# Kernel tuning notes

Measured on AMD Instinct MI355X. Metric: run time of the kernel, lower is better.

The kernel has to match this reference:

```python
import jax, jax.numpy as jnp
import numpy as np

D = 64       # CNF state dimension
H = 512      # MLP hidden width
B = 8192     # batch


def setup_inputs() -> dict:
    key = jax.random.key(0)
    ks = jax.random.split(key, 8)
    s1 = 1.0 / np.sqrt(D + 1)
    s2 = 1.0 / np.sqrt(H)
    return {
        "t": jax.random.uniform(ks[0], (1,), dtype=jnp.float32),
        "x": jax.random.normal(ks[1], (B, D + 1), dtype=jnp.float32),
        "W1": jax.random.normal(ks[2], (D + 1, H), dtype=jnp.float32) * s1,
        "b1": jnp.zeros((H,), dtype=jnp.float32),
        "W2": jax.random.normal(ks[3], (H, H), dtype=jnp.float32) * s2,
        "b2": jnp.zeros((H,), dtype=jnp.float32),
        "W3": jax.random.normal(ks[4], (H, D), dtype=jnp.float32) * s2,
        "b3": jnp.zeros((D,), dtype=jnp.float32),
    }


def reference(t, x, W1, b1, W2, b2, W3, b3):
    # CNF.forward: strip log-density channel, evaluate vf and its exact divergence.
    xs = x[..., :-1]                      # [B, D]
    tt = t[0]

    def vf_single(xi):                    # xi: [D] -> [D]
        inp = jnp.concatenate([tt[None], xi])          # vf(t*ones, x) with t prepended
        h = jnp.tanh(inp @ W1 + b1)
        h = jnp.tanh(h @ W2 + b2)
        return h @ W3 + b3

    dx = jax.vmap(vf_single)(xs)                        # [B, D]
    # exact divergence: trace of per-sample Jacobian via reverse-mode (matches torch jacrev)
    J = jax.vmap(jax.jacrev(vf_single))(xs)             # [B, D, D]
    div = jnp.trace(J, axis1=-2, axis2=-1)              # [B]
    return jnp.concatenate([dx, div[:, None]], axis=-1) # [B, D+1]
```

## Files before the change

kernel.cpp:

```cpp
#include <hip/hip_runtime.h>

#define HH 512
#define DD 64
#define MROWS 32
#define TPB 512
#define LP 520

typedef unsigned short u16;
typedef short s16x8 __attribute__((ext_vector_type(8)));
typedef float f32x4 __attribute__((ext_vector_type(4)));

#define MFMA16(A,B,C) __builtin_amdgcn_mfma_f32_16x16x32_bf16((A),(B),(C),0,0,0)

#define OFF_W2K  0
#define OFF_EFK  262144
#define OFF_W1F  524288
#define OFF_W3F  557056
#define OFF_Z0B  (589824 * 2)

__device__ __forceinline__ u16 f2bf(float f) {
    unsigned u = __builtin_bit_cast(unsigned, f);
    u += 0x7fffu + ((u >> 16) & 1u);
    return (u16)(u >> 16);
}
__device__ __forceinline__ float bf2f(u16 h) {
    return __builtin_bit_cast(float, (unsigned)h << 16);
}
__device__ __forceinline__ float fast_tanh(float x) {
    float e = __expf(2.0f * x);
    return 1.0f - 2.0f * __builtin_amdgcn_rcpf(e + 1.0f);
}
__device__ __forceinline__ void gll(const u16* g, u16* l) {
    __builtin_amdgcn_global_load_lds(
        (const __attribute__((address_space(1))) unsigned int*)g,
        (__attribute__((address_space(3))) unsigned int*)l, 16, 0, 0);
}
__device__ __forceinline__ void wait_vm4() {
    asm volatile("s_waitcnt vmcnt(4)" ::: "memory");
}
__device__ __forceinline__ void wait_vm0() {
    asm volatile("s_waitcnt vmcnt(0)" ::: "memory");
}
__device__ __forceinline__ void fence_lds_reads() {
    asm volatile("s_waitcnt lgkmcnt(0)" ::: "memory");
}

__global__ __launch_bounds__(256) void precompute(
    const float* __restrict__ t,  const float* __restrict__ W1,
    const float* __restrict__ b1, const float* __restrict__ W2,
    const float* __restrict__ W3, u16* __restrict__ ws16, float* __restrict__ z0)
{
    __shared__ float T[16 * 264 > 256 * 20 ? 16 * 264 : 256 * 20];
    u16* W2K = ws16 + OFF_W2K;
    u16* EFK = ws16 + OFF_EFK;
    u16* W1F = ws16 + OFF_W1F;
    u16* W3F = ws16 + OFF_W3F;

    const int bid = blockIdx.x, tid = threadIdx.x;
    const int lane = tid & 63, wv = tid >> 6;
    const int m16 = lane & 15, q = lane >> 4;

    if (bid < 64) {
        const int nt = bid >> 1, bh = bid & 1;
        const int a0 = nt * 16, b0 = bh * 256;
        s16x8 afh[2], afl[2];
#pragma unroll
        for (int h = 0; h < 2; ++h)
#pragma unroll
            for (int j = 0; j < 8; ++j) {
                int i = h * 32 + q * 8 + j;
                float v = W1[(1 + i) * HH + a0 + m16];
                u16 hi = f2bf(v);
                afh[h][j] = (short)hi;
                afl[h][j] = (short)f2bf(v - bf2f(hi));
            }
#pragma unroll
        for (int bt = 0; bt < 4; ++bt) {
            int bl = wv * 64 + bt * 16;
            s16x8 bfh[2], bfl[2];
#pragma unroll
            for (int h = 0; h < 2; ++h) {
                const float* src = W3 + (b0 + bl + m16) * DD + h * 32 + q * 8;
                float4 p0 = *(const float4*)(src);
                float4 p1 = *(const float4*)(src + 4);
                float vv[8] = {p0.x,p0.y,p0.z,p0.w,p1.x,p1.y,p1.z,p1.w};
#pragma unroll
                for (int j = 0; j < 8; ++j) {
                    u16 hi = f2bf(vv[j]);
                    bfh[h][j] = (short)hi;
                    bfl[h][j] = (short)f2bf(vv[j] - bf2f(hi));
                }
            }
            f32x4 c = {0.f, 0.f, 0.f, 0.f};
#pragma unroll
            for (int h = 0; h < 2; ++h) {
                c = MFMA16(afh[h], bfh[h], c);
                c = MFMA16(afh[h], bfl[h], c);
                c = MFMA16(afl[h], bfh[h], c);
            }
#pragma unroll
            for (int r = 0; r < 4; ++r)
                T[(4 * q + r) * 264 + bl + m16] = c[r];
        }
        __syncthreads();
#pragma unroll
        for (int p = 0; p < 2; ++p) {
            int ksl = p * 4 + wv;
            int al  = m16;
            int blc = ksl * 32 + q * 8;
            const float* w2p = W2 + (a0 + al) * HH + b0 + blc;
            float4 wa = *(const float4*)(w2p), wb = *(const float4*)(w2p + 4);
            const float* glp = T + al * 264 + blc;
            s16x8 o;
            o[0]=(short)f2bf(wa.x*glp[0]); o[1]=(short)f2bf(wa.y*glp[1]);
            o[2]=(short)f2bf(wa.z*glp[2]); o[3]=(short)f2bf(wa.w*glp[3]);
            o[4]=(short)f2bf(wb.x*glp[4]); o[5]=(short)f2bf(wb.y*glp[5]);
            o[6]=(short)f2bf(wb.z*glp[6]); o[7]=(short)f2bf(wb.w*glp[7]);
            *(s16x8*)(EFK + (b0 / 32 + ksl) * 16384 + nt * 512 + lane * 8) = o;
        }
        if (bh == 0 && tid < 128) {
            int ks = tid >> 6, ln = tid & 63;
            int n  = nt * 16 + (ln & 15);
            int k0 = ks * 32 + (ln >> 4) * 8;
            s16x8 o;
#pragma unroll
            for (int j = 0; j < 8; ++j) o[j] = (short)f2bf(W1[(1 + k0 + j) * HH + n]);
            *(s16x8*)(W1F + nt * 1024 + ks * 512 + ln * 8) = o;
        }
    } else if (bid < 128) {
        const int nt = (bid - 64) >> 1, kh = (bid - 64) & 1;
        const int n0 = nt * 16, k0 = kh * 256;
#pragma unroll
        for (int it = 0; it < 4; ++it) {
            int r = (tid >> 2) + it * 64;
            int c = (tid & 3) * 4;
            float4 v = *(const float4*)(W2 + (k0 + r) * HH + n0 + c);
            *(float4*)(T + r * 20 + c) = v;
        }
        __syncthreads();
#pragma unroll
        for (int p = 0; p < 2; ++p) {
            int ksl = p * 4 + wv;
            int kqx = ksl * 32 + q * 8;
            s16x8 o;
#pragma unroll
            for (int j = 0; j < 8; ++j) o[j] = (short)f2bf(T[(kqx + j) * 20 + m16]);
            *(s16x8*)(W2K + (k0 / 32 + ksl) * 16384 + nt * 512 + lane * 8) = o;
        }
    } else if (bid < 136) {
        const int ot = (bid - 128) >> 1, kh = (bid - 128) & 1;
        const int o0 = ot * 16, k0 = kh * 256;
#pragma unroll
        for (int it = 0; it < 4; ++it) {
            int r = (tid >> 2) + it * 64;
            int c = (tid & 3) * 4;
            float4 v = *(const float4*)(W3 + (k0 + r) * DD + o0 + c);
            *(float4*)(T + r * 20 + c) = v;
        }
        __syncthreads();
#pragma unroll
        for (int p = 0; p < 2; ++p) {
            int ksl = p * 4 + wv;
            int kqx = ksl * 32 + q * 8;
            s16x8 o;
#pragma unroll
            for (int j = 0; j < 8; ++j) o[j] = (short)f2bf(T[(kqx + j) * 20 + m16]);
            *(s16x8*)(W3F + ot * 8192 + (k0 / 32 + ksl) * 512 + lane * 8) = o;
        }
    } else {
        for (int n = tid; n < HH; n += 256)
            z0[n] = b1[n] + t[0] * W1[n];
    }
}

__global__ __launch_bounds__(TPB) void cnf_main(
    const float* __restrict__ x,  const u16* __restrict__ ws16,
    const float* __restrict__ z0, const float* __restrict__ b2,
    const float* __restrict__ b3, float* __restrict__ out)
{
    __shared__ u16 h1s[MROWS * LP];
    __shared__ u16 h2s[MROWS * LP];
    __shared__ u16 stg[2][16384];
    __shared__ float z0s[HH];
    __shared__ float b2s[HH];
    __shared__ float b3s[DD];
    __shared__ float divacc[8][MROWS];

    const u16* W2K = ws16 + OFF_W2K;
    const u16* EFK = ws16 + OFF_EFK;
    const u16* W1F = ws16 + OFF_W1F;
    const u16* W3F = ws16 + OFF_W3F;

    const int tid  = threadIdx.x;
    const int lane = tid & 63;
    const int w    = tid >> 6;
    const int m16  = lane & 15;
    const int q    = lane >> 4;
    const int kq   = q * 8;
    const int r0   = blockIdx.x * MROWS;

    u16* xs = h2s;

#pragma unroll
    for (int j = 0; j < 4; ++j)
        gll(W2K + (4 * w + j) * 512 + lane * 8,         stg[0] + w * 2048 + j * 512);
#pragma unroll
    for (int j = 0; j < 4; ++j)
        gll(W2K + 16384 + (4 * w + j) * 512 + lane * 8, stg[1] + w * 2048 + j * 512);

    for (int idx = tid; idx < MROWS * DD; idx += TPB) {
        int r = idx >> 6, c = idx & 63;
        xs[r * 72 + c] = f2bf(x[(r0 + r) * (DD + 1) + c]);
    }
    z0s[tid] = z0[tid];
    b2s[tid] = b2[tid];
    if (tid < DD) b3s[tid] = b3[tid];

    s16x8 b1f[4][2];
#pragma unroll
    for (int j = 0; j < 4; ++j) {
        const u16* bb = W1F + (4 * w + j) * 1024 + lane * 8;
        b1f[j][0] = *(const s16x8*)(bb);
        b1f[j][1] = *(const s16x8*)(bb + 512);
    }
    __syncthreads();

    float d1reg[2][4][4];

    {
        s16x8 xa[2][2];
#pragma unroll
        for (int rt = 0; rt < 2; ++rt) {
            xa[rt][0] = *(const s16x8*)(xs + (rt * 16 + m16) * 72 + kq);
            xa[rt][1] = *(const s16x8*)(xs + (rt * 16 + m16) * 72 + 32 + kq);
        }
#pragma unroll
        for (int j = 0; j < 4; ++j) {
            int col = (4 * w + j) * 16 + m16;
#pragma unroll
            for (int rt = 0; rt < 2; ++rt) {
                f32x4 c = {0.f, 0.f, 0.f, 0.f};
                c = MFMA16(xa[rt][0], b1f[j][0], c);
                c = MFMA16(xa[rt][1], b1f[j][1], c);
#pragma unroll
                for (int i = 0; i < 4; ++i) {
                    float hv = fast_tanh(c[i] + z0s[col]);
                    h1s[(rt * 16 + 4 * q + i) * LP + col] = f2bf(hv);
                    d1reg[rt][j][i] = 1.0f - hv * hv;
                }
            }
        }
    }
    __syncthreads();

    f32x4 acc[2][4];
#pragma unroll
    for (int rt = 0; rt < 2; ++rt)
#pragma unroll
        for (int j = 0; j < 4; ++j) acc[rt][j] = f32x4{0.f,0.f,0.f,0.f};
    {
        const u16* ap0 = h1s + m16 * LP + kq;
        const u16* ap1 = h1s + (16 + m16) * LP + kq;
#pragma unroll 4
        for (int c = 0; c < 16; ++c) {
            if (c < 15) wait_vm4(); else wait_vm0();
            u16* sb = stg[c & 1] + w * 2048;
            s16x8 bf0 = *(const s16x8*)(sb +        lane * 8);
            s16x8 bf1 = *(const s16x8*)(sb +  512 + lane * 8);
            s16x8 bf2 = *(const s16x8*)(sb + 1024 + lane * 8);
            s16x8 bf3 = *(const s16x8*)(sb + 1536 + lane * 8);
            s16x8 f0  = *(const s16x8*)(ap0 + c * 32);
            s16x8 f1  = *(const s16x8*)(ap1 + c * 32);
            acc[0][0] = MFMA16(f0, bf0, acc[0][0]);
            acc[1][0] = MFMA16(f1, bf0, acc[1][0]);
            acc[0][1] = MFMA16(f0, bf1, acc[0][1]);
            acc[1][1] = MFMA16(f1, bf1, acc[1][1]);
            acc[0][2] = MFMA16(f0, bf2, acc[0][2]);
            acc[1][2] = MFMA16(f1, bf2, acc[1][2]);
            acc[0][3] = MFMA16(f0, bf3, acc[0][3]);
            acc[1][3] = MFMA16(f1, bf3, acc[1][3]);
            if (c < 14) {
                fence_lds_reads();
                const u16* src = W2K + (c + 2) * 16384 + 4 * w * 512 + lane * 8;
#pragma unroll
                for (int j = 0; j < 4; ++j) gll(src + j * 512, sb + j * 512);
            }
        }
    }

    fence_lds_reads();
#pragma unroll
    for (int j = 0; j < 4; ++j)
        gll(EFK + (4 * w + j) * 512 + lane * 8,         stg[0] + w * 2048 + j * 512);
#pragma unroll
    for (int j = 0; j < 4; ++j)
        gll(EFK + 16384 + (4 * w + j) * 512 + lane * 8, stg[1] + w * 2048 + j * 512);

#pragma unroll
    for (int j = 0; j < 4; ++j) {
        int col = (4 * w + j) * 16 + m16;
#pragma unroll
        for (int rt = 0; rt < 2; ++rt)
#pragma unroll
            for (int i = 0; i < 4; ++i)
                h2s[(rt * 16 + 4 * q + i) * LP + col] =
                    f2bf(fast_tanh(acc[rt][j][i] + b2s[col]));
    }
    __syncthreads();

    {
        const int rowt = w >> 2, ot = w & 3;
        const u16* ap = h2s + (rowt * 16 + m16) * LP + kq;
        const u16* bp = W3F + ot * 8192 + lane * 8;
        s16x8 W3r[4];
#pragma unroll
        for (int k = 0; k < 4; ++k) W3r[k] = *(const s16x8*)(bp + k * 512);
        f32x4 cA = {0.f,0.f,0.f,0.f}, cB = {0.f,0.f,0.f,0.f};
#pragma unroll
        for (int c = 0; c < 16; ++c) {
            s16x8 f = *(const s16x8*)(ap + c * 32);
            const int sl = c & 3;
            if (c & 1) cB = MFMA16(f, W3r[sl], cB);
            else       cA = MFMA16(f, W3r[sl], cA);
            if (c < 12) W3r[sl] = *(const s16x8*)(bp + (c + 4) * 512);
        }
        f32x4 c3 = cA + cB;
        int o = ot * 16 + m16;
#pragma unroll
        for (int i = 0; i < 4; ++i)
            out[(r0 + rowt * 16 + 4 * q + i) * (DD + 1) + o] = c3[i] + b3s[o];
    }

    {
        f32x4 g[2][4];
#pragma unroll
        for (int rt = 0; rt < 2; ++rt)
#pragma unroll
            for (int j = 0; j < 4; ++j) g[rt][j] = f32x4{0.f,0.f,0.f,0.f};
        const u16* ap0 = h2s + m16 * LP + kq;
        const u16* ap1 = h2s + (16 + m16) * LP + kq;
#pragma unroll 4
        for (int c = 0; c < 16; ++c) {
            if (c < 15) wait_vm4(); else wait_vm0();
            u16* sb = stg[c & 1] + w * 2048;
            s16x8 ef0 = *(const s16x8*)(sb +        lane * 8);
            s16x8 ef1 = *(const s16x8*)(sb +  512 + lane * 8);
            s16x8 ef2 = *(const s16x8*)(sb + 1024 + lane * 8);
            s16x8 ef3 = *(const s16x8*)(sb + 1536 + lane * 8);
            s16x8 hf0 = *(const s16x8*)(ap0 + c * 32);
            s16x8 hf1 = *(const s16x8*)(ap1 + c * 32);
            s16x8 af0, af1;
#pragma unroll
            for (int jj = 0; jj < 8; ++jj) {
                float v0 = bf2f((u16)hf0[jj]);
                float v1 = bf2f((u16)hf1[jj]);
                af0[jj] = (short)f2bf(1.0f - v0 * v0);
                af1[jj] = (short)f2bf(1.0f - v1 * v1);
            }
            g[0][0] = MFMA16(af0, ef0, g[0][0]);
            g[1][0] = MFMA16(af1, ef0, g[1][0]);
            g[0][1] = MFMA16(af0, ef1, g[0][1]);
            g[1][1] = MFMA16(af1, ef1, g[1][1]);
            g[0][2] = MFMA16(af0, ef2, g[0][2]);
            g[1][2] = MFMA16(af1, ef2, g[1][2]);
            g[0][3] = MFMA16(af0, ef3, g[0][3]);
            g[1][3] = MFMA16(af1, ef3, g[1][3]);
            if (c < 14) {
                fence_lds_reads();
                const u16* src = EFK + (c + 2) * 16384 + 4 * w * 512 + lane * 8;
#pragma unroll
                for (int j = 0; j < 4; ++j) gll(src + j * 512, sb + j * 512);
            }
        }
#pragma unroll
        for (int rt = 0; rt < 2; ++rt)
#pragma unroll
            for (int i = 0; i < 4; ++i) {
                float v = d1reg[rt][0][i] * g[rt][0][i]
                        + d1reg[rt][1][i] * g[rt][1][i]
                        + d1reg[rt][2][i] * g[rt][2][i]
                        + d1reg[rt][3][i] * g[rt][3][i];
                v += __shfl_xor(v, 1, 64);
                v += __shfl_xor(v, 2, 64);
                v += __shfl_xor(v, 4, 64);
                v += __shfl_xor(v, 8, 64);
                if (m16 == 0) divacc[w][rt * 16 + 4 * q + i] = v;
            }
    }
    __syncthreads();

    if (tid < MROWS) {
        float s = 0.0f;
#pragma unroll
        for (int ww = 0; ww < 8; ++ww) s += divacc[ww][tid];
        out[(r0 + tid) * (DD + 1) + DD] = s;
    }
}

extern "C" void kernel_launch(void* const* d_in, const int* in_sizes, int n_in,
                              void* d_out, int out_size, void* d_ws, size_t ws_size,
                              hipStream_t stream) {
    const float* t  = (const float*)d_in[0];
    const float* x  = (const float*)d_in[1];
    const float* W1 = (const float*)d_in[2];
    const float* b1 = (const float*)d_in[3];
    const float* W2 = (const float*)d_in[4];
    const float* b2 = (const float*)d_in[5];
    const float* W3 = (const float*)d_in[6];
    const float* b3 = (const float*)d_in[7];
    float* out = (float*)d_out;

    u16*   ws16 = (u16*)d_ws;
    float* z0   = (float*)((char*)d_ws + OFF_Z0B);

    precompute<<<137, 256, 0, stream>>>(t, W1, b1, W2, W3, ws16, z0);
    cnf_main<<<8192 / MROWS, TPB, 0, stream>>>(x, ws16, z0, b2, b3, out);
}
```

Before: 96.82 us.

## Split fused CNF kernel into four staged kernels with larger GEMM tiles

The single fused kernel is replaced by four kernels: layer-1 (writing h1 and d1 to workspace in MFMA-fragment layout), a 128x128-tiled W2 GEMM producing h2 and its tanh derivative, a 128x128-tiled divergence GEMM against EFK, and an output kernel for W3 that also sums the partial divergences. Larger tiles are meant to raise weight reuse, since each 32-row block previously streamed all of W2 and EFK. The cost is extra launches and global round-trips of intermediates (h1, h2, d2, d1), roughly tens of MB of traffic, plus less per-block parallelism with only 256 blocks of 256 threads.

```diff
diff --git a/kernel.cpp b/kernel.cpp
--- a/kernel.cpp
+++ b/kernel.cpp
@@ -2,9 +2,6 @@
 
 #define HH 512
 #define DD 64
-#define MROWS 32
-#define TPB 512
-#define LP 520
 
 typedef unsigned short u16;
 typedef short s16x8 __attribute__((ext_vector_type(8)));
@@ -17,6 +14,11 @@
 #define OFF_W1F  524288
 #define OFF_W3F  557056
 #define OFF_Z0B  (589824 * 2)
+#define OFF_H1T_B (2u*1024*1024)
+#define OFF_H2T_B (12u*1024*1024)
+#define OFF_D2T_B (22u*1024*1024)
+#define OFF_D1_B  (32u*1024*1024)
+#define OFF_PD_B  (42u*1024*1024)
 
 __device__ __forceinline__ u16 f2bf(float f) {
     unsigned u = __builtin_bit_cast(unsigned, f);
@@ -34,15 +36,6 @@
     __builtin_amdgcn_global_load_lds(
         (const __attribute__((address_space(1))) unsigned int*)g,
         (__attribute__((address_space(3))) unsigned int*)l, 16, 0, 0);
-}
-__device__ __forceinline__ void wait_vm4() {
-    asm volatile("s_waitcnt vmcnt(4)" ::: "memory");
-}
-__device__ __forceinline__ void wait_vm0() {
-    asm volatile("s_waitcnt vmcnt(0)" ::: "memory");
-}
-__device__ __forceinline__ void fence_lds_reads() {
-    asm volatile("s_waitcnt lgkmcnt(0)" ::: "memory");
 }
 
 __global__ __launch_bounds__(256) void precompute(
@@ -173,49 +166,24 @@
     }
 }
 
-__global__ __launch_bounds__(TPB) void cnf_main(
-    const float* __restrict__ x,  const u16* __restrict__ ws16,
-    const float* __restrict__ z0, const float* __restrict__ b2,
-    const float* __restrict__ b3, float* __restrict__ out)
+__global__ __launch_bounds__(512) void k1_h1(
+    const float* __restrict__ x, const u16* __restrict__ ws16,
+    const float* __restrict__ z0, u16* __restrict__ h1t, u16* __restrict__ d1)
 {
-    __shared__ u16 h1s[MROWS * LP];
-    __shared__ u16 h2s[MROWS * LP];
-    __shared__ u16 stg[2][16384];
+    __shared__ u16 h1s[32 * 520];
+    __shared__ u16 xs[32 * 72];
     __shared__ float z0s[HH];
-    __shared__ float b2s[HH];
-    __shared__ float b3s[DD];
-    __shared__ float divacc[8][MROWS];
-
-    const u16* W2K = ws16 + OFF_W2K;
-    const u16* EFK = ws16 + OFF_EFK;
+
     const u16* W1F = ws16 + OFF_W1F;
-    const u16* W3F = ws16 + OFF_W3F;
-
-    const int tid  = threadIdx.x;
-    const int lane = tid & 63;
-    const int w    = tid >> 6;
-    const int m16  = lane & 15;
-    const int q    = lane >> 4;
-    const int kq   = q * 8;
-    const int r0   = blockIdx.x * MROWS;
-
-    u16* xs = h2s;
-
-#pragma unroll
-    for (int j = 0; j < 4; ++j)
-        gll(W2K + (4 * w + j) * 512 + lane * 8,         stg[0] + w * 2048 + j * 512);
-#pragma unroll
-    for (int j = 0; j < 4; ++j)
-        gll(W2K + 16384 + (4 * w + j) * 512 + lane * 8, stg[1] + w * 2048 + j * 512);
-
-    for (int idx = tid; idx < MROWS * DD; idx += TPB) {
+    const int tid = threadIdx.x, lane = tid & 63, w = tid >> 6;
+    const int m16 = lane & 15, q = lane >> 4, kq = q * 8;
+    const int r0 = blockIdx.x * 32;
+
+    for (int idx = tid; idx < 32 * DD; idx += 512) {
         int r = idx >> 6, c = idx & 63;
         xs[r * 72 + c] = f2bf(x[(r0 + r) * (DD + 1) + c]);
     }
     z0s[tid] = z0[tid];
-    b2s[tid] = b2[tid];
-    if (tid < DD) b3s[tid] = b3[tid];
-
     s16x8 b1f[4][2];
 #pragma unroll
     for (int j = 0; j < 4; ++j) {
@@ -225,8 +193,6 @@
     }
     __syncthreads();
 
-    float d1reg[2][4][4];
-
     {
         s16x8 xa[2][2];
 #pragma unroll
@@ -245,155 +211,225 @@
 #pragma unroll
                 for (int i = 0; i < 4; ++i) {
                     float hv = fast_tanh(c[i] + z0s[col]);
-                    h1s[(rt * 16 + 4 * q + i) * LP + col] = f2bf(hv);
-                    d1reg[rt][j][i] = 1.0f - hv * hv;
+                    h1s[(rt * 16 + 4 * q + i) * 520 + col] = f2bf(hv);
+                    d1[(r0 + rt * 16 + 4 * q + i) * HH + col] = f2bf(1.0f - hv * hv);
                 }
             }
         }
     }
     __syncthreads();
 
-    f32x4 acc[2][4];
-#pragma unroll
-    for (int rt = 0; rt < 2; ++rt)
-#pragma unroll
-        for (int j = 0; j < 4; ++j) acc[rt][j] = f32x4{0.f,0.f,0.f,0.f};
-    {
-        const u16* ap0 = h1s + m16 * LP + kq;
-        const u16* ap1 = h1s + (16 + m16) * LP + kq;
-#pragma unroll 4
-        for (int c = 0; c < 16; ++c) {
-            if (c < 15) wait_vm4(); else wait_vm0();
-            u16* sb = stg[c & 1] + w * 2048;
-            s16x8 bf0 = *(const s16x8*)(sb +        lane * 8);
-            s16x8 bf1 = *(const s16x8*)(sb +  512 + lane * 8);
-            s16x8 bf2 = *(const s16x8*)(sb + 1024 + lane * 8);
-            s16x8 bf3 = *(const s16x8*)(sb + 1536 + lane * 8);
-            s16x8 f0  = *(const s16x8*)(ap0 + c * 32);
-            s16x8 f1  = *(const s16x8*)(ap1 + c * 32);
-            acc[0][0] = MFMA16(f0, bf0, acc[0][0]);
-            acc[1][0] = MFMA16(f1, bf0, acc[1][0]);
-            acc[0][1] = MFMA16(f0, bf1, acc[0][1]);
-            acc[1][1] = MFMA16(f1, bf1, acc[1][1]);
-            acc[0][2] = MFMA16(f0, bf2, acc[0][2]);
-            acc[1][2] = MFMA16(f1, bf2, acc[1][2]);
-            acc[0][3] = MFMA16(f0, bf3, acc[0][3]);
-            acc[1][3] = MFMA16(f1, bf3, acc[1][3]);
-            if (c < 14) {
-                fence_lds_reads();
-                const u16* src = W2K + (c + 2) * 16384 + 4 * w * 512 + lane * 8;
-#pragma unroll
-                for (int j = 0; j < 4; ++j) gll(src + j * 512, sb + j * 512);
-            }
-        }
-    }
-
-    fence_lds_reads();
-#pragma unroll
-    for (int j = 0; j < 4; ++j)
-        gll(EFK + (4 * w + j) * 512 + lane * 8,         stg[0] + w * 2048 + j * 512);
-#pragma unroll
-    for (int j = 0; j < 4; ++j)
-        gll(EFK + 16384 + (4 * w + j) * 512 + lane * 8, stg[1] + w * 2048 + j * 512);
-
-#pragma unroll
-    for (int j = 0; j < 4; ++j) {
-        int col = (4 * w + j) * 16 + m16;
-#pragma unroll
-        for (int rt = 0; rt < 2; ++rt)
-#pragma unroll
-            for (int i = 0; i < 4; ++i)
-                h2s[(rt * 16 + 4 * q + i) * LP + col] =
-                    f2bf(fast_tanh(acc[rt][j][i] + b2s[col]));
+    const int rowblk = blockIdx.x >> 2;
+#pragma unroll
+    for (int p = 0; p < 2; ++p) {
+        int ch = 2 * w + p;
+#pragma unroll
+        for (int rt = 0; rt < 2; ++rt) {
+            int rtg = (blockIdx.x & 3) * 2 + rt;
+            s16x8 f = *(const s16x8*)(h1s + (rt * 16 + m16) * 520 + ch * 32 + kq);
+            *(s16x8*)(h1t + (rowblk * 16 + ch) * 4096 + rtg * 512 + lane * 8) = f;
+        }
+    }
+}
+
+__global__ __launch_bounds__(256) void k2_h2(
+    const u16* __restrict__ ws16, const u16* __restrict__ h1t,
+    const float* __restrict__ b2, u16* __restrict__ h2t, u16* __restrict__ d2t)
+{
+    __shared__ u16 smem[16384];
+
+    const u16* W2K = ws16 + OFF_W2K;
+    const int tid = threadIdx.x, lane = tid & 63, w = tid >> 6;
+    const int m16 = lane & 15, q = lane >> 4, kq = q * 8;
+    const int rowblk = blockIdx.x >> 2, ng = blockIdx.x & 3;
+    const int rh = w >> 1, nh = w & 1;
+
+    const u16* habase = h1t + rowblk * 16 * 4096;
+
+#pragma unroll
+    for (int s = 0; s < 2; ++s) {
+        gll(habase + (w + 4 * s) * 512 + lane * 8, smem + (w + 4 * s) * 512);
+        gll(W2K + (ng * 8 + w + 4 * s) * 512 + lane * 8, smem + 4096 + (w + 4 * s) * 512);
     }
     __syncthreads();
 
-    {
-        const int rowt = w >> 2, ot = w & 3;
-        const u16* ap = h2s + (rowt * 16 + m16) * LP + kq;
-        const u16* bp = W3F + ot * 8192 + lane * 8;
-        s16x8 W3r[4];
-#pragma unroll
-        for (int k = 0; k < 4; ++k) W3r[k] = *(const s16x8*)(bp + k * 512);
-        f32x4 cA = {0.f,0.f,0.f,0.f}, cB = {0.f,0.f,0.f,0.f};
-#pragma unroll
-        for (int c = 0; c < 16; ++c) {
-            s16x8 f = *(const s16x8*)(ap + c * 32);
-            const int sl = c & 3;
-            if (c & 1) cB = MFMA16(f, W3r[sl], cB);
-            else       cA = MFMA16(f, W3r[sl], cA);
-            if (c < 12) W3r[sl] = *(const s16x8*)(bp + (c + 4) * 512);
-        }
-        f32x4 c3 = cA + cB;
-        int o = ot * 16 + m16;
-#pragma unroll
-        for (int i = 0; i < 4; ++i)
-            out[(r0 + rowt * 16 + 4 * q + i) * (DD + 1) + o] = c3[i] + b3s[o];
-    }
-
-    {
-        f32x4 g[2][4];
-#pragma unroll
-        for (int rt = 0; rt < 2; ++rt)
-#pragma unroll
-            for (int j = 0; j < 4; ++j) g[rt][j] = f32x4{0.f,0.f,0.f,0.f};
-        const u16* ap0 = h2s + m16 * LP + kq;
-        const u16* ap1 = h2s + (16 + m16) * LP + kq;
-#pragma unroll 4
-        for (int c = 0; c < 16; ++c) {
-            if (c < 15) wait_vm4(); else wait_vm0();
-            u16* sb = stg[c & 1] + w * 2048;
-            s16x8 ef0 = *(const s16x8*)(sb +        lane * 8);
-            s16x8 ef1 = *(const s16x8*)(sb +  512 + lane * 8);
-            s16x8 ef2 = *(const s16x8*)(sb + 1024 + lane * 8);
-            s16x8 ef3 = *(const s16x8*)(sb + 1536 + lane * 8);
-            s16x8 hf0 = *(const s16x8*)(ap0 + c * 32);
-            s16x8 hf1 = *(const s16x8*)(ap1 + c * 32);
-            s16x8 af0, af1;
-#pragma unroll
-            for (int jj = 0; jj < 8; ++jj) {
-                float v0 = bf2f((u16)hf0[jj]);
-                float v1 = bf2f((u16)hf1[jj]);
-                af0[jj] = (short)f2bf(1.0f - v0 * v0);
-                af1[jj] = (short)f2bf(1.0f - v1 * v1);
-            }
-            g[0][0] = MFMA16(af0, ef0, g[0][0]);
-            g[1][0] = MFMA16(af1, ef0, g[1][0]);
-            g[0][1] = MFMA16(af0, ef1, g[0][1]);
-            g[1][1] = MFMA16(af1, ef1, g[1][1]);
-            g[0][2] = MFMA16(af0, ef2, g[0][2]);
-            g[1][2] = MFMA16(af1, ef2, g[1][2]);
-            g[0][3] = MFMA16(af0, ef3, g[0][3]);
-            g[1][3] = MFMA16(af1, ef3, g[1][3]);
-            if (c < 14) {
-                fence_lds_reads();
-                const u16* src = EFK + (c + 2) * 16384 + 4 * w * 512 + lane * 8;
-#pragma unroll
-                for (int j = 0; j < 4; ++j) gll(src + j * 512, sb + j * 512);
-            }
-        }
-#pragma unroll
-        for (int rt = 0; rt < 2; ++rt)
-#pragma unroll
-            for (int i = 0; i < 4; ++i) {
-                float v = d1reg[rt][0][i] * g[rt][0][i]
-                        + d1reg[rt][1][i] * g[rt][1][i]
-                        + d1reg[rt][2][i] * g[rt][2][i]
-                        + d1reg[rt][3][i] * g[rt][3][i];
-                v += __shfl_xor(v, 1, 64);
-                v += __shfl_xor(v, 2, 64);
-                v += __shfl_xor(v, 4, 64);
-                v += __shfl_xor(v, 8, 64);
-                if (m16 == 0) divacc[w][rt * 16 + 4 * q + i] = v;
-            }
+    f32x4 acc[4][4];
+#pragma unroll
+    for (int rt = 0; rt < 4; ++rt)
+#pragma unroll
+        for (int nt = 0; nt < 4; ++nt) acc[rt][nt] = f32x4{0.f, 0.f, 0.f, 0.f};
+
+    for (int c = 0; c < 16; ++c) {
+        u16* cur = smem + (c & 1) * 8192;
+        if (c < 15) {
+            u16* nxt = smem + ((c + 1) & 1) * 8192;
+#pragma unroll
+            for (int s = 0; s < 2; ++s) {
+                gll(habase + (c + 1) * 4096 + (w + 4 * s) * 512 + lane * 8,
+                    nxt + (w + 4 * s) * 512);
+                gll(W2K + (c + 1) * 16384 + (ng * 8 + w + 4 * s) * 512 + lane * 8,
+                    nxt + 4096 + (w + 4 * s) * 512);
+            }
+        }
+        s16x8 af[4], bf[4];
+#pragma unroll
+        for (int t = 0; t < 4; ++t) {
+            af[t] = *(const s16x8*)(cur + (rh * 4 + t) * 512 + lane * 8);
+            bf[t] = *(const s16x8*)(cur + 4096 + (nh * 4 + t) * 512 + lane * 8);
+        }
+#pragma unroll
+        for (int rt = 0; rt < 4; ++rt)
+#pragma unroll
+            for (int nt = 0; nt < 4; ++nt)
+                acc[rt][nt] = MFMA16(af[rt], bf[nt], acc[rt][nt]);
+        __syncthreads();
+    }
+
+    float b2v[4];
+#pragma unroll
+    for (int nt = 0; nt < 4; ++nt)
+        b2v[nt] = b2[ng * 128 + (nh * 4 + nt) * 16 + m16];
+
+    for (int hh = 0; hh < 2; ++hh) {
+        if (rh == hh) {
+#pragma unroll
+            for (int rt = 0; rt < 4; ++rt)
+#pragma unroll
+                for (int nt = 0; nt < 4; ++nt)
+#pragma unroll
+                    for (int i = 0; i < 4; ++i)
+                        smem[(rt * 16 + 4 * q + i) * 136 + (nh * 4 + nt) * 16 + m16] =
+                            f2bf(fast_tanh(acc[rt][nt][i] + b2v[nt]));
+        }
+        __syncthreads();
+#pragma unroll
+        for (int chl = 0; chl < 4; ++chl) {
+            s16x8 h = *(const s16x8*)(smem + (w * 16 + m16) * 136 + chl * 32 + kq);
+            s16x8 d;
+#pragma unroll
+            for (int j = 0; j < 8; ++j) {
+                float hv = bf2f((u16)h[j]);
+                d[j] = (short)f2bf(1.0f - hv * hv);
+            }
+            int addr = (rowblk * 16 + ng * 4 + chl) * 4096 + (hh * 4 + w) * 512 + lane * 8;
+            *(s16x8*)(h2t + addr) = h;
+            *(s16x8*)(d2t + addr) = d;
+        }
+        __syncthreads();
+    }
+}
+
+__global__ __launch_bounds__(256) void k4_div(
+    const u16* __restrict__ ws16, const u16* __restrict__ d2t,
+    const u16* __restrict__ d1, float* __restrict__ pd)
+{
+    __shared__ u16 smem[16384];
+    __shared__ float divacc[2][128];
+
+    const u16* EFK = ws16 + OFF_EFK;
+    const int tid = threadIdx.x, lane = tid & 63, w = tid >> 6;
+    const int m16 = lane & 15, q = lane >> 4;
+    const int rowblk = blockIdx.x >> 2, ng = blockIdx.x & 3;
+    const int rh = w >> 1, nh = w & 1;
+
+    const u16* dabase = d2t + rowblk * 16 * 4096;
+
+#pragma unroll
+    for (int s = 0; s < 2; ++s) {
+        gll(dabase + (w + 4 * s) * 512 + lane * 8, smem + (w + 4 * s) * 512);
+        gll(EFK + (ng * 8 + w + 4 * s) * 512 + lane * 8, smem + 4096 + (w + 4 * s) * 512);
     }
     __syncthreads();
 
-    if (tid < MROWS) {
-        float s = 0.0f;
-#pragma unroll
-        for (int ww = 0; ww < 8; ++ww) s += divacc[ww][tid];
-        out[(r0 + tid) * (DD + 1) + DD] = s;
+    f32x4 acc[4][4];
+#pragma unroll
+    for (int rt = 0; rt < 4; ++rt)
+#pragma unroll
+        for (int nt = 0; nt < 4; ++nt) acc[rt][nt] = f32x4{0.f, 0.f, 0.f, 0.f};
+
+    for (int c = 0; c < 16; ++c) {
+        u16* cur = smem + (c & 1) * 8192;
+        if (c < 15) {
+            u16* nxt = smem + ((c + 1) & 1) * 8192;
+#pragma unroll
+            for (int s = 0; s < 2; ++s) {
+                gll(dabase + (c + 1) * 4096 + (w + 4 * s) * 512 + lane * 8,
+                    nxt + (w + 4 * s) * 512);
+                gll(EFK + (c + 1) * 16384 + (ng * 8 + w + 4 * s) * 512 + lane * 8,
+                    nxt + 4096 + (w + 4 * s) * 512);
+            }
+        }
+        s16x8 af[4], bf[4];
+#pragma unroll
+        for (int t = 0; t < 4; ++t) {
+            af[t] = *(const s16x8*)(cur + (rh * 4 + t) * 512 + lane * 8);
+            bf[t] = *(const s16x8*)(cur + 4096 + (nh * 4 + t) * 512 + lane * 8);
+        }
+#pragma unroll
+        for (int rt = 0; rt < 4; ++rt)
+#pragma unroll
+            for (int nt = 0; nt < 4; ++nt)
+                acc[rt][nt] = MFMA16(af[rt], bf[nt], acc[rt][nt]);
+        __syncthreads();
+    }
+
+#pragma unroll
+    for (int rt = 0; rt < 4; ++rt)
+#pragma unroll
+        for (int i = 0; i < 4; ++i) {
+            int row = rowblk * 128 + (rh * 4 + rt) * 16 + 4 * q + i;
+            float v = 0.0f;
+#pragma unroll
+            for (int nt = 0; nt < 4; ++nt) {
+                int col = ng * 128 + (nh * 4 + nt) * 16 + m16;
+                v += bf2f(d1[row * HH + col]) * acc[rt][nt][i];
+            }
+            v += __shfl_xor(v, 1, 64);
+            v += __shfl_xor(v, 2, 64);
+            v += __shfl_xor(v, 4, 64);
+            v += __shfl_xor(v, 8, 64);
+            if (m16 == 0) divacc[nh][(rh * 4 + rt) * 16 + 4 * q + i] = v;
+        }
+    __syncthreads();
+    if (tid < 128)
+        pd[ng * 8192 + rowblk * 128 + tid] = divacc[0][tid] + divacc[1][tid];
+}
+
+__global__ __launch_bounds__(512) void k3_out(
+    const u16* __restrict__ ws16, const u16* __restrict__ h2t,
+    const float* __restrict__ b3, const float* __restrict__ pd,
+    float* __restrict__ out)
+{
+    const u16* W3F = ws16 + OFF_W3F;
+    const int tid = threadIdx.x, lane = tid & 63, w = tid >> 6;
+    const int m16 = lane & 15, q = lane >> 4;
+    const int r0 = blockIdx.x * 32;
+    const int rowblk = blockIdx.x >> 2;
+    const int rtl = w >> 2, ot = w & 3;
+    const int rtg = (blockIdx.x & 3) * 2 + rtl;
+
+    const u16* ap = h2t + rowblk * 16 * 4096 + rtg * 512 + lane * 8;
+    const u16* bp = W3F + ot * 8192 + lane * 8;
+
+    f32x4 cA = {0.f,0.f,0.f,0.f}, cB = {0.f,0.f,0.f,0.f};
+#pragma unroll
+    for (int c = 0; c < 16; ++c) {
+        s16x8 a = *(const s16x8*)(ap + c * 4096);
+        s16x8 b = *(const s16x8*)(bp + c * 512);
+        if (c & 1) cB = MFMA16(a, b, cB);
+        else       cA = MFMA16(a, b, cA);
+    }
+    f32x4 c3 = cA + cB;
+    int o = ot * 16 + m16;
+    float b3v = b3[o];
+#pragma unroll
+    for (int i = 0; i < 4; ++i)
+        out[(r0 + rtl * 16 + 4 * q + i) * (DD + 1) + o] = c3[i] + b3v;
+
+    if (tid < 32) {
+        int gr = r0 + tid;
+        out[gr * (DD + 1) + DD] =
+            pd[gr] + pd[8192 + gr] + pd[16384 + gr] + pd[24576 + gr];
     }
 }
 
@@ -412,7 +448,15 @@
 
     u16*   ws16 = (u16*)d_ws;
     float* z0   = (float*)((char*)d_ws + OFF_Z0B);
+    u16*   h1t  = (u16*)((char*)d_ws + OFF_H1T_B);
+    u16*   h2t  = (u16*)((char*)d_ws + OFF_H2T_B);
+    u16*   d2t  = (u16*)((char*)d_ws + OFF_D2T_B);
+    u16*   d1   = (u16*)((char*)d_ws + OFF_D1_B);
+    float* pd   = (float*)((char*)d_ws + OFF_PD_B);
 
     precompute<<<137, 256, 0, stream>>>(t, W1, b1, W2, W3, ws16, z0);
-    cnf_main<<<8192 / MROWS, TPB, 0, stream>>>(x, ws16, z0, b2, b3, out);
-}
+    k1_h1<<<256, 512, 0, stream>>>(x, ws16, z0, h1t, d1);
+    k2_h2<<<256, 256, 0, stream>>>(ws16, h1t, b2, h2t, d2t);
+    k4_div<<<256, 256, 0, stream>>>(ws16, d2t, d1, pd);
+    k3_out<<<256, 512, 0, stream>>>(ws16, h2t, b3, pd, out);
+}
```

New measurement: 119.1 us. 1.23x slower.
